# Optimization experiments

Hardware: AMD Instinct MI355X
Metric: run time of the kernel (lower is better)

The kernel has to match this reference:

```python
import math
import jax, jax.numpy as jnp
import numpy as np

IN_CH = 1
K = 2       # kernel_size
S = 2       # stride (== K, non-overlapping)
P = 0       # padding
NQ = 4      # num_qubits = IN_CH*K*K
NL = 2      # num_qreps (StronglyEntanglingLayers n_layers)


def setup_inputs() -> dict:
    key = jax.random.key(0)
    k1, k2 = jax.random.split(key)
    x = jax.random.normal(k1, (64, 1, 224, 224), dtype=jnp.float32)
    # PennyLane TorchLayer default init: uniform(0, 2*pi)
    weights = jax.random.uniform(k2, (NL, NQ, 3), dtype=jnp.float32,
                                 minval=0.0, maxval=2.0 * math.pi)
    return {"x": x, "weights": weights}


def _apply_1q(state, gate, q, n):
    # state: (B, 2**n) complex; apply 2x2 gate on wire q (wire 0 = MSB).
    B = state.shape[0]
    st = state.reshape(B, 2 ** q, 2, -1)
    st = jnp.einsum('ab,xlbr->xlar', gate, st)
    return st.reshape(B, -1)


def _cnot(state, ctrl, tgt, n):
    # CNOT(ctrl, tgt): flip target bit where control bit == 1.
    B = state.shape[0]
    st = state.reshape((B,) + (2,) * n)
    ax_c = 1 + ctrl
    ax_t = 1 + tgt
    s0 = jnp.take(st, 0, axis=ax_c)
    s1 = jnp.take(st, 1, axis=ax_c)
    ax_t_after = ax_t - 1 if ax_t > ax_c else ax_t
    s1 = jnp.flip(s1, axis=ax_t_after)  # X on target
    st = jnp.stack([s0, s1], axis=ax_c)
    return st.reshape(B, -1)


def _rot_gate(phi, theta, omega):
    # qml.Rot(phi, theta, omega) = RZ(omega) @ RY(theta) @ RZ(phi)
    a = 0.5 * (phi + omega)
    b = 0.5 * (phi - omega)
    ct = jnp.cos(0.5 * theta)
    st = jnp.sin(0.5 * theta)
    ep = jnp.exp(-1j * a)  # e^{-i(phi+omega)/2}
    em = jnp.exp(1j * b)   # e^{+i(phi-omega)/2}
    return jnp.stack([jnp.stack([ep * ct, -em * st]),
                      jnp.stack([jnp.conj(em) * st, jnp.conj(ep) * ct])])


def _run_circuit(flat, weights):
    # flat: (B, NQ) real angles; weights: (NL, NQ, 3).
    # AngleEmbedding(rotation='Y') on |0..0>: product state of [cos(x/2), sin(x/2)].
    B = flat.shape[0]
    n = NQ
    half = 0.5 * flat
    ca = jnp.cos(half)
    sa = jnp.sin(half)
    state = jnp.ones((B, 1), jnp.float32)
    for q in range(n):
        amp = jnp.stack([ca[:, q], sa[:, q]], axis=-1)  # (B, 2)
        state = (state[:, :, None] * amp[:, None, :]).reshape(B, -1)
    state = state.astype(jnp.complex64)
    # StronglyEntanglingLayers: per layer, Rot on each wire then ring of CNOTs
    # with range r = (l % (n-1)) + 1.
    n_layers = weights.shape[0]
    for l in range(n_layers):
        for q in range(n):
            g = _rot_gate(weights[l, q, 0], weights[l, q, 1], weights[l, q, 2])
            state = _apply_1q(state, g, q, n)
        r = (l % (n - 1)) + 1
        for q in range(n):
            state = _cnot(state, q, (q + r) % n, n)
    probs = (state.real ** 2 + state.imag ** 2).reshape((B,) + (2,) * n)
    # <Z_i> = P(bit_i = 0) - P(bit_i = 1)
    z = [(jnp.take(probs, 0, axis=1 + i) - jnp.take(probs, 1, axis=1 + i))
         .reshape(B, -1).sum(-1) for i in range(n)]
    return jnp.stack(z, axis=-1)  # (B, NQ)


def reference(x, weights):
    b, c, H, W = x.shape
    # stride == kernel_size, padding == 0 -> non-overlapping patches via reshape
    ho = (H - K) // S + 1
    wo = (W - K) // S + 1
    patches = x.reshape(b, c, ho, K, wo, K).transpose(0, 1, 2, 4, 3, 5)
    flat = patches.reshape(-1, c * K * K)            # (B, NQ), torch unfold order
    flat = jnp.tanh(flat) * (math.pi / 2.0)
    q = _run_circuit(flat, weights)                   # (B, NQ)
    qm = q.reshape(b, ho, wo, NQ)
    return qm.transpose(0, 3, 1, 2)                   # (b, NQ, ho, wo)
```

## Files before the change

### kernel.cpp

```cpp
#include <hip/hip_runtime.h>
#include <math.h>

#define DIM 16

__global__ __launch_bounds__(256) void quanv_precompute(const float* __restrict__ w,
                                                        float* __restrict__ C) {
  __shared__ float Ur[DIM][20];
  __shared__ float Ui[DIM][20];
  __shared__ float Ad[4][DIM][DIM];
  const int tid = threadIdx.x;

  if (tid < DIM) {
    float ur[DIM], ui[DIM];
#pragma unroll
    for (int m = 0; m < DIM; ++m) { ur[m] = (m == tid) ? 1.0f : 0.0f; ui[m] = 0.0f; }
#pragma unroll
    for (int l = 0; l < 2; ++l) {
#pragma unroll
      for (int q = 0; q < 4; ++q) {
        const float phi = w[l * 12 + q * 3 + 0];
        const float th  = w[l * 12 + q * 3 + 1];
        const float om  = w[l * 12 + q * 3 + 2];
        const float a  = 0.5f * (phi + om);
        const float bb = 0.5f * (phi - om);
        float ct, st, ca, sa, cb, sb;
        __sincosf(0.5f * th, &st, &ct);
        __sincosf(a, &sa, &ca);
        __sincosf(bb, &sb, &cb);
        const float g00r =  ca * ct, g00i = -sa * ct;
        const float g01r = -cb * st, g01i = -sb * st;
        const float g10r =  cb * st, g10i = -sb * st;
        const float g11r =  ca * ct, g11i =  sa * ct;
        const int bit = 1 << (3 - q);
#pragma unroll
        for (int m = 0; m < DIM; ++m) {
          if (m & bit) continue;
          const int m1 = m | bit;
          const float v0r = ur[m],  v0i = ui[m];
          const float v1r = ur[m1], v1i = ui[m1];
          ur[m]  = g00r * v0r - g00i * v0i + g01r * v1r - g01i * v1i;
          ui[m]  = g00r * v0i + g00i * v0r + g01r * v1i + g01i * v1r;
          ur[m1] = g10r * v0r - g10i * v0i + g11r * v1r - g11i * v1i;
          ui[m1] = g10r * v0i + g10i * v0r + g11r * v1i + g11i * v1r;
        }
      }
      const int r = (l % 3) + 1;
#pragma unroll
      for (int q = 0; q < 4; ++q) {
        const int cbit = 1 << (3 - q);
        const int tbit = 1 << (3 - ((q + r) & 3));
#pragma unroll
        for (int m = 0; m < DIM; ++m) {
          if ((m & cbit) && !(m & tbit)) {
            const int m1 = m | tbit;
            float t;
            t = ur[m]; ur[m] = ur[m1]; ur[m1] = t;
            t = ui[m]; ui[m] = ui[m1]; ui[m1] = t;
          }
        }
      }
    }
#pragma unroll
    for (int m = 0; m < DIM; ++m) { Ur[tid][m] = ur[m]; Ui[tid][m] = ui[m]; }
  }
  __syncthreads();

  {
    const int j = tid >> 4, k = tid & 15;
    float term[DIM];
#pragma unroll
    for (int m = 0; m < DIM; ++m)
      term[m] = Ur[j][m] * Ur[k][m] + Ui[j][m] * Ui[k][m];
#pragma unroll
    for (int i = 0; i < 4; ++i) {
      float s = 0.0f;
#pragma unroll
      for (int m = 0; m < DIM; ++m)
        s += ((m >> (3 - i)) & 1) ? -term[m] : term[m];
      Ad[i][j][k] = s;
    }
  }
  __syncthreads();

  for (int idx = tid; idx < 4 * 81; idx += 256) {
    const int i = idx / 81;
    const int rr = idx - i * 81;
    const int v0 = rr / 27, v1 = (rr / 9) % 3, v2 = (rr / 3) % 3, v3 = rr % 3;
    float s = 0.0f;
#pragma unroll
    for (int b = 0; b < 16; ++b) {
      const int b0 = (b >> 3) & 1, b1 = (b >> 2) & 1, b2 = (b >> 1) & 1, b3 = b & 1;
      const int k0 = (v0 == 2) ? (b0 ^ 1) : b0;
      const int k1 = (v1 == 2) ? (b1 ^ 1) : b1;
      const int k2 = (v2 == 2) ? (b2 ^ 1) : b2;
      const int k3 = (v3 == 2) ? (b3 ^ 1) : b3;
      const int neg = (((v0 == 1) & b0) ^ ((v1 == 1) & b1) ^
                       ((v2 == 1) & b2) ^ ((v3 == 1) & b3));
      const int k = (k0 << 3) | (k1 << 2) | (k2 << 1) | k3;
      const float term = Ad[i][b][k];
      s += neg ? -term : term;
    }
    C[idx] = 0.0625f * s;
  }
}

static __device__ __forceinline__ void pix_trig(float xx, float& c, float& s) {
  xx = fminf(10.0f, fmaxf(-10.0f, xx));
  const float u = __expf(xx + xx);
  const float th = (u - 1.0f) * __builtin_amdgcn_rcpf(u + 1.0f);
  __sincosf(th * 1.57079632679489662f, &s, &c);
}

__global__ __launch_bounds__(256) void quanv_main(const float* __restrict__ x,
                                                  const float* __restrict__ C,
                                                  float* __restrict__ out) {
  const int idx = blockIdx.x * 256 + threadIdx.x;
  const int b   = idx / 12544;
  const int rem = idx - b * 12544;
  const int i   = rem / 112;
  const int j   = rem - i * 112;

  const float* px = x + (size_t)b * 50176 + (size_t)(2 * i) * 224 + 2 * j;
  const float2 r0 = *(const float2*)(px);
  const float2 r1 = *(const float2*)(px + 224);

  float c0, s0, c1, s1, c2, s2, c3, s3;
  pix_trig(r0.x, c0, s0);
  pix_trig(r0.y, c1, s1);
  pix_trig(r1.x, c2, s2);
  pix_trig(r1.y, c3, s3);

  const float g0v[3] = {1.0f, c0, s0};
  const float g1v[3] = {1.0f, c1, s1};
  const float g2v[3] = {1.0f, c2, s2};

  float o[4];
#pragma unroll
  for (int oi = 0; oi < 4; ++oi) {
    const float* D = C + oi * 81;
    float acc0 = 0.0f;
#pragma unroll
    for (int v0 = 0; v0 < 3; ++v0) {
      float acc1 = 0.0f;
#pragma unroll
      for (int v1 = 0; v1 < 3; ++v1) {
        float acc2 = 0.0f;
#pragma unroll
        for (int v2 = 0; v2 < 3; ++v2) {
          const int base = ((v0 * 3 + v1) * 3 + v2) * 3;
          float t = fmaf(s3, D[base + 2], fmaf(c3, D[base + 1], D[base + 0]));
          acc2 = (v2 == 0) ? t : fmaf(g2v[v2], t, acc2);
        }
        acc1 = (v1 == 0) ? acc2 : fmaf(g1v[v1], acc2, acc1);
      }
      acc0 = (v0 == 0) ? acc1 : fmaf(g0v[v0], acc1, acc0);
    }
    o[oi] = acc0;
  }

  float* po = out + (size_t)b * 4 * 12544 + (size_t)i * 112 + j;
  po[0 * 12544] = o[0];
  po[1 * 12544] = o[1];
  po[2 * 12544] = o[2];
  po[3 * 12544] = o[3];
}

extern "C" void kernel_launch(void* const* d_in, const int* in_sizes, int n_in,
                              void* d_out, int out_size, void* d_ws, size_t ws_size,
                              hipStream_t stream) {
  const float* x = (const float*)d_in[0];
  const float* w = (const float*)d_in[1];
  float* out = (float*)d_out;
  float* C   = (float*)d_ws;

  quanv_precompute<<<1, 256, 0, stream>>>(w, C);
  quanv_main<<<3136, 256, 0, stream>>>(x, C, out);
}
```

Measured before the change: 23.66 us.

## Fuse coefficient precompute into main kernel with four pixels per thread

Removes the separate single-block precompute launch by having every block recompute the 16x16 unitary and the 324 polynomial coefficients into shared memory, then evaluate four pixels per thread. This drops one kernel launch and the serial dependency on a one-block kernel. The cost is redundant precompute work in each of 784 blocks, including a 16-thread serial section, extra barriers, and higher register pressure from holding four pixels' state.

```diff
diff --git a/kernel.cpp b/kernel.cpp
--- a/kernel.cpp
+++ b/kernel.cpp
@@ -3,11 +3,20 @@
 
 #define DIM 16
 
-__global__ __launch_bounds__(256) void quanv_precompute(const float* __restrict__ w,
-                                                        float* __restrict__ C) {
+static __device__ __forceinline__ void pix_trig(float xx, float& c, float& s) {
+  xx = fminf(10.0f, fmaxf(-10.0f, xx));
+  const float u = __expf(xx + xx);
+  const float th = (u - 1.0f) * __builtin_amdgcn_rcpf(u + 1.0f);
+  __sincosf(th * 1.57079632679489662f, &s, &c);
+}
+
+__global__ __launch_bounds__(256) void quanv_fused(const float* __restrict__ x,
+                                                   const float* __restrict__ w,
+                                                   float* __restrict__ out) {
   __shared__ float Ur[DIM][20];
   __shared__ float Ui[DIM][20];
   __shared__ float Ad[4][DIM][DIM];
+  __shared__ float Cs[4 * 81];
   const int tid = threadIdx.x;
 
   if (tid < DIM) {
@@ -100,69 +109,64 @@
       const float term = Ad[i][b][k];
       s += neg ? -term : term;
     }
-    C[idx] = 0.0625f * s;
+    Cs[idx] = 0.0625f * s;
   }
-}
+  __syncthreads();
 
-static __device__ __forceinline__ void pix_trig(float xx, float& c, float& s) {
-  xx = fminf(10.0f, fmaxf(-10.0f, xx));
-  const float u = __expf(xx + xx);
-  const float th = (u - 1.0f) * __builtin_amdgcn_rcpf(u + 1.0f);
-  __sincosf(th * 1.57079632679489662f, &s, &c);
-}
+  const int base_pid = blockIdx.x * 1024 + tid;
+  float g0[4][3], g1[4][3], g2[4][3], c3a[4], s3a[4];
+  int obase[4];
+#pragma unroll
+  for (int p = 0; p < 4; ++p) {
+    const int pid = base_pid + p * 256;
+    const int b   = pid / 12544;
+    const int rem = pid - b * 12544;
+    const int i   = rem / 112;
+    const int j   = rem - i * 112;
+    const float* px = x + (size_t)b * 50176 + (size_t)(2 * i) * 224 + 2 * j;
+    const float2 r0 = *(const float2*)(px);
+    const float2 r1 = *(const float2*)(px + 224);
+    float c0, s0, c1, s1, c2, s2, c3, s3;
+    pix_trig(r0.x, c0, s0);
+    pix_trig(r0.y, c1, s1);
+    pix_trig(r1.x, c2, s2);
+    pix_trig(r1.y, c3, s3);
+    g0[p][0] = 1.0f; g0[p][1] = c0; g0[p][2] = s0;
+    g1[p][0] = 1.0f; g1[p][1] = c1; g1[p][2] = s1;
+    g2[p][0] = 1.0f; g2[p][1] = c2; g2[p][2] = s2;
+    c3a[p] = c3; s3a[p] = s3;
+    obase[p] = b * 50176 + i * 112 + j;
+  }
 
-__global__ __launch_bounds__(256) void quanv_main(const float* __restrict__ x,
-                                                  const float* __restrict__ C,
-                                                  float* __restrict__ out) {
-  const int idx = blockIdx.x * 256 + threadIdx.x;
-  const int b   = idx / 12544;
-  const int rem = idx - b * 12544;
-  const int i   = rem / 112;
-  const int j   = rem - i * 112;
-
-  const float* px = x + (size_t)b * 50176 + (size_t)(2 * i) * 224 + 2 * j;
-  const float2 r0 = *(const float2*)(px);
-  const float2 r1 = *(const float2*)(px + 224);
-
-  float c0, s0, c1, s1, c2, s2, c3, s3;
-  pix_trig(r0.x, c0, s0);
-  pix_trig(r0.y, c1, s1);
-  pix_trig(r1.x, c2, s2);
-  pix_trig(r1.y, c3, s3);
-
-  const float g0v[3] = {1.0f, c0, s0};
-  const float g1v[3] = {1.0f, c1, s1};
-  const float g2v[3] = {1.0f, c2, s2};
-
-  float o[4];
 #pragma unroll
   for (int oi = 0; oi < 4; ++oi) {
-    const float* D = C + oi * 81;
-    float acc0 = 0.0f;
+    float a0[4], a1[4], a2[4];
 #pragma unroll
     for (int v0 = 0; v0 < 3; ++v0) {
-      float acc1 = 0.0f;
 #pragma unroll
       for (int v1 = 0; v1 < 3; ++v1) {
-        float acc2 = 0.0f;
 #pragma unroll
         for (int v2 = 0; v2 < 3; ++v2) {
-          const int base = ((v0 * 3 + v1) * 3 + v2) * 3;
-          float t = fmaf(s3, D[base + 2], fmaf(c3, D[base + 1], D[base + 0]));
-          acc2 = (v2 == 0) ? t : fmaf(g2v[v2], t, acc2);
+          const int base = oi * 81 + ((v0 * 3 + v1) * 3 + v2) * 3;
+          const float d0 = Cs[base], d1 = Cs[base + 1], d2 = Cs[base + 2];
+#pragma unroll
+          for (int p = 0; p < 4; ++p) {
+            const float t = fmaf(s3a[p], d2, fmaf(c3a[p], d1, d0));
+            a2[p] = (v2 == 0) ? t : fmaf(g2[p][v2], t, a2[p]);
+          }
         }
-        acc1 = (v1 == 0) ? acc2 : fmaf(g1v[v1], acc2, acc1);
+#pragma unroll
+        for (int p = 0; p < 4; ++p)
+          a1[p] = (v1 == 0) ? a2[p] : fmaf(g1[p][v1], a2[p], a1[p]);
       }
-      acc0 = (v0 == 0) ? acc1 : fmaf(g0v[v0], acc1, acc0);
+#pragma unroll
+      for (int p = 0; p < 4; ++p)
+        a0[p] = (v0 == 0) ? a1[p] : fmaf(g0[p][v0], a1[p], a0[p]);
     }
-    o[oi] = acc0;
+#pragma unroll
+    for (int p = 0; p < 4; ++p)
+      out[obase[p] + oi * 12544] = a0[p];
   }
-
-  float* po = out + (size_t)b * 4 * 12544 + (size_t)i * 112 + j;
-  po[0 * 12544] = o[0];
-  po[1 * 12544] = o[1];
-  po[2 * 12544] = o[2];
-  po[3 * 12544] = o[3];
 }
 
 extern "C" void kernel_launch(void* const* d_in, const int* in_sizes, int n_in,
@@ -171,8 +175,6 @@
   const float* x = (const float*)d_in[0];
   const float* w = (const float*)d_in[1];
   float* out = (float*)d_out;
-  float* C   = (float*)d_ws;
 
-  quanv_precompute<<<1, 256, 0, stream>>>(w, C);
-  quanv_main<<<3136, 256, 0, stream>>>(x, C, out);
+  quanv_fused<<<784, 256, 0, stream>>>(x, w, out);
 }
```

New measurement: 27.13 us. 14.7% more time.
